# Optimization experiments

Hardware: AMD Instinct MI355X
Metric: run time of the kernel (lower is better)

The kernel has to match this reference:

```python
import jax, jax.numpy as jnp
import numpy as np

B, T, D, H = 4, 2048, 1024, 16
DK = DV = 64
R = 64
KS = 4
EPS = 1e-6


def setup_inputs() -> dict:
    key = jax.random.key(0)
    ks = jax.random.split(key, 16)
    def w(k, shape, s=0.02):
        return jax.random.normal(k, shape, jnp.float32) * s
    return {
        "x": jax.random.normal(ks[0], (B, T, D), jnp.float32),
        "conv_q_w": w(ks[1], (D, 1, KS), 0.3), "conv_q_b": jnp.zeros((D,), jnp.float32),
        "conv_k_w": w(ks[2], (D, 1, KS), 0.3), "conv_k_b": jnp.zeros((D,), jnp.float32),
        "conv_v_w": w(ks[3], (D, 1, KS), 0.3), "conv_v_b": jnp.zeros((D,), jnp.float32),
        "Wq": w(ks[4], (D, H * DK)), "bq": jnp.zeros((H * DK,), jnp.float32),
        "Wk": w(ks[5], (D, H * DK)), "bk": jnp.zeros((H * DK,), jnp.float32),
        "Wv": w(ks[6], (D, H * DV)), "bv": jnp.zeros((H * DV,), jnp.float32),
        "W_ad": w(ks[7], (D, R)), "b_ad": jnp.zeros((R,), jnp.float32),
        "W_au": w(ks[8], (R, H * DK)), "b_au": jnp.zeros((H * DK,), jnp.float32),
        "W_beta": w(ks[9], (D, H)), "b_beta": jnp.zeros((H,), jnp.float32),
        "rms_w": jnp.ones((H, DV), jnp.float32),
        "W_gd": w(ks[10], (D, R)), "b_gd": jnp.zeros((R,), jnp.float32),
        "W_gu": w(ks[11], (R, H)), "b_gu": jnp.zeros((H,), jnp.float32),
        "Wo": w(ks[12], (H * DV, D)), "bo": jnp.zeros((D,), jnp.float32),
    }


def _shortconv(x, w, b):
    # causal depthwise conv1d: torch pads (KS-1) both sides then slices [:T] == left-pad KS-1
    xc = jnp.transpose(x, (0, 2, 1))  # [B, D, T]
    y = jax.lax.conv_general_dilated(
        xc, w, (1,), [(KS - 1, 0)],
        dimension_numbers=("NCH", "OIH", "NCH"), feature_group_count=D)
    y = y + b[None, :, None]
    return jax.nn.silu(jnp.transpose(y, (0, 2, 1)))  # [B, T, D]


def _l2(x):
    # x / sqrt(clamp(sum(x^2), eps))  (matches torch clamp_min then sqrt)
    return x / jnp.sqrt(jnp.maximum(jnp.sum(x * x, -1, keepdims=True), EPS))


def _heads(z, dh):
    # [B,T,H*dh] -> [B*H,T,dh]
    return jnp.transpose(z.reshape(B, T, H, dh), (0, 2, 1, 3)).reshape(B * H, T, dh)


def reference(x, conv_q_w, conv_q_b, conv_k_w, conv_k_b, conv_v_w, conv_v_b,
              Wq, bq, Wk, bk, Wv, bv, W_ad, b_ad, W_au, b_au, W_beta, b_beta,
              rms_w, W_gd, b_gd, W_gu, b_gu, Wo, bo):
    qx = _shortconv(x, conv_q_w, conv_q_b)
    kx = _shortconv(x, conv_k_w, conv_k_b)
    vx = _shortconv(x, conv_v_w, conv_v_b)
    Q = _l2(_heads(qx @ Wq + bq, DK))            # [BH,T,DK]
    K = _l2(_heads(kx @ Wk + bk, DK))            # [BH,T,DK]
    V = _heads(vx @ Wv + bv, DV)                 # [BH,T,DV]
    alpha = jax.nn.sigmoid(jax.nn.silu(x @ W_ad + b_ad) @ W_au + b_au)  # [B,T,H*DK]
    A = _heads(alpha, DK)                        # [BH,T,DK]
    beta = jax.nn.sigmoid(x @ W_beta + b_beta)   # [B,T,H]
    Bta = jnp.transpose(beta, (0, 2, 1)).reshape(B * H, T, 1)

    S0 = jnp.zeros((B * H, DK, DV), jnp.float32)

    def step(S, inp):
        q, k, v, a, b = inp                      # [BH,DK],[BH,DK],[BH,DV],[BH,DK],[BH,1]
        S = S * a[:, :, None]                    # gated decay (row scale)
        kTS = jnp.einsum("bi,bij->bj", k, S)    # k^T S : [BH,DV]
        S = S + (b * k)[:, :, None] * (v - kTS)[:, None, :]  # rank-1 delta update
        o = jnp.einsum("bij,bi->bj", S, q)      # S^T q : [BH,DV]
        return S, o

    tm = lambda z: jnp.transpose(z, (1, 0, 2))   # time-major for scan
    S_final, out_t = jax.lax.scan(step, S0, (tm(Q), tm(K), tm(V), tm(A), tm(Bta)))
    O = jnp.transpose(out_t, (1, 0, 2)).reshape(B, H, T, DV)

    # headwise RMSNorm then sigmoid output gate
    var = jnp.mean(O * O, -1, keepdims=True)
    O = O * jax.lax.rsqrt(var + EPS) * rms_w[None, :, None, :]
    gate = jax.nn.sigmoid(jax.nn.silu(x @ W_gd + b_gd) @ W_gu + b_gu)  # [B,T,H]
    O = O * jnp.transpose(gate, (0, 2, 1))[:, :, :, None]

    y = jnp.transpose(O, (0, 2, 1, 3)).reshape(B, T, H * DV) @ Wo + bo
    return y, S_final.reshape(B, H, DK, DV)
```

## Files before the change

### kernel.cpp

```cpp
#include <hip/hip_runtime.h>
#include <hip/hip_bf16.h>
#include <cstdint>

#define BB 4
#define TT 2048
#define DD 1024
#define HH 16
#define NR (BB*TT)
#define CC 16
#define NCH (TT/CC)

typedef __attribute__((ext_vector_type(8))) short bf16x8;
typedef __attribute__((ext_vector_type(4))) float f32x4;
typedef __attribute__((ext_vector_type(2))) float f32x2;
typedef __attribute__((ext_vector_type(4))) unsigned int u32x4;
typedef __attribute__((ext_vector_type(2))) unsigned int u32x2;

#define GLL(g, l, SZ) __builtin_amdgcn_global_load_lds( \
    (const __attribute__((address_space(1))) void*)(uintptr_t)(const void*)(g), \
    (__attribute__((address_space(3))) void*)(uintptr_t)(void*)(l), SZ, 0, 0)

__device__ __forceinline__ unsigned short f2bf(float f) {
  unsigned u = __builtin_bit_cast(unsigned, f);
  unsigned r = 0x7FFFu + ((u >> 16) & 1u);
  return (unsigned short)((u + r) >> 16);
}
__device__ __forceinline__ unsigned pk2(float a, float b) {
  return (unsigned)f2bf(a) | ((unsigned)f2bf(b) << 16);
}
__device__ __forceinline__ float siluf(float v) { return v / (1.f + __expf(-v)); }
__device__ __forceinline__ float sigmf(float v) { return 1.f / (1.f + __expf(-v)); }


__global__ __launch_bounds__(256) void transpose_convert(
    const float* __restrict__ W, unsigned short* __restrict__ Wt, int K, int N) {
  __shared__ float tile[64][65];
  const int tid = threadIdx.x;
  const int bk = blockIdx.x * 64, bn = blockIdx.y * 64;
  const int r = tid >> 2, c4 = (tid & 3) * 16;
#pragma unroll 4
  for (int e = 0; e < 16; ++e)
    tile[r][c4 + e] = W[(size_t)(bk + r) * N + bn + c4 + e];
  __syncthreads();
#pragma unroll 4
  for (int e = 0; e < 16; ++e)
    Wt[(size_t)(bn + r) * K + bk + c4 + e] = f2bf(tile[c4 + e][r]);
}

__global__ void conv_small_T(const float* __restrict__ W, unsigned short* __restrict__ Wt,
                             int K, int N, int Npad) {
  int idx = blockIdx.x * 256 + threadIdx.x;
  if (idx >= Npad * K) return;
  int n = idx / K, k = idx - n * K;
  float v = (n < N) ? W[(size_t)k * N + n] : 0.f;
  Wt[idx] = f2bf(v);
}

__global__ void pack_stage1_T(const float* __restrict__ Wad, const float* __restrict__ Wgd,
                              const float* __restrict__ Wbeta, unsigned short* __restrict__ Wt) {
  int idx = blockIdx.x * 256 + threadIdx.x;
  int n = idx >> 10, k = idx & 1023;
  float v = 0.f;
  if (n < 64) v = Wad[(size_t)k * 64 + n];
  else if (n < 128) v = Wgd[(size_t)k * 64 + (n - 64)];
  else if (n < 144) v = Wbeta[(size_t)k * 16 + (n - 128)];
  Wt[idx] = f2bf(v);
}

__global__ void pack_bias(const float* __restrict__ bad, const float* __restrict__ bgd,
                          const float* __restrict__ bbeta, const float* __restrict__ bgu,
                          float* __restrict__ bst1, float* __restrict__ bgup) {
  int t = threadIdx.x;
  float v = 0.f;
  if (t < 64) v = bad[t];
  else if (t < 128) v = bgd[t - 64];
  else if (t < 144) v = bbeta[t - 128];
  bst1[t] = v;
  if (t < 128) bgup[t] = (t < 16) ? bgu[t] : 0.f;
}

__global__ __launch_bounds__(256) void conv_silu(
    const float* __restrict__ x,
    const float* __restrict__ qw, const float* __restrict__ qb,
    const float* __restrict__ kw, const float* __restrict__ kb,
    const float* __restrict__ vw, const float* __restrict__ vb,
    unsigned short* __restrict__ qx, unsigned short* __restrict__ kx,
    unsigned short* __restrict__ vx, unsigned short* __restrict__ xb) {
  const int n = blockIdx.x;
  const int t = n & (TT - 1);
  const int d0 = threadIdx.x * 4;
  const size_t base = (size_t)n * DD + d0;
  f32x4 zero = {0.f, 0.f, 0.f, 0.f};
  f32x4 x0 = *(const f32x4*)(x + base);
  f32x4 xm1 = (t >= 1) ? *(const f32x4*)(x + base - DD) : zero;
  f32x4 xm2 = (t >= 2) ? *(const f32x4*)(x + base - 2 * DD) : zero;
  f32x4 xm3 = (t >= 3) ? *(const f32x4*)(x + base - 3 * DD) : zero;
  float sq[4], sk[4], sv[4];
#pragma unroll
  for (int e = 0; e < 4; ++e) {
    const int d = d0 + e;
    const f32x4 wq = *(const f32x4*)(qw + (size_t)d * 4);
    const f32x4 wk = *(const f32x4*)(kw + (size_t)d * 4);
    const f32x4 wv = *(const f32x4*)(vw + (size_t)d * 4);
    float aq = wq[0] * xm3[e] + wq[1] * xm2[e] + wq[2] * xm1[e] + wq[3] * x0[e] + qb[d];
    float ak = wk[0] * xm3[e] + wk[1] * xm2[e] + wk[2] * xm1[e] + wk[3] * x0[e] + kb[d];
    float av = wv[0] * xm3[e] + wv[1] * xm2[e] + wv[2] * xm1[e] + wv[3] * x0[e] + vb[d];
    sq[e] = siluf(aq); sk[e] = siluf(ak); sv[e] = siluf(av);
  }
  u32x2 o;
  o[0] = pk2(sq[0], sq[1]); o[1] = pk2(sq[2], sq[3]); *(u32x2*)(qx + base) = o;
  o[0] = pk2(sk[0], sk[1]); o[1] = pk2(sk[2], sk[3]); *(u32x2*)(kx + base) = o;
  o[0] = pk2(sv[0], sv[1]); o[1] = pk2(sv[2], sv[3]); *(u32x2*)(vx + base) = o;
  o[0] = pk2(x0[0], x0[1]); o[1] = pk2(x0[2], x0[3]); *(u32x2*)(xb + base) = o;
}

template <int ACT>
__global__ __launch_bounds__(256) void gemm_bt(
    const unsigned short* __restrict__ A, const unsigned short* __restrict__ Bt,
    const float* __restrict__ bias, float* __restrict__ C,
    int M, int N, int K, int ldc, int nstore) {
  __shared__ unsigned short lsA[128 * 32];
  __shared__ unsigned short lsB[128 * 32];
  const int tid = threadIdx.x;
  const int wid = tid >> 6, lane = tid & 63;
  const int wr = wid >> 1, wc = wid & 1;
  const int m0 = blockIdx.x * 128, n0 = blockIdx.y * 128;
  f32x4 acc[4][4] = {};
  const int nk = K >> 5;
  const int r0 = wid * 32 + (lane >> 2);
  const int cb = (lane & 3) * 16;
  char* lA = (char*)lsA;
  char* lB = (char*)lsB;
  const size_t rowb = (size_t)K * 2;

  for (int kt = 0; kt < nk; ++kt) {
    const char* gA = (const char*)(A + (size_t)(m0 + r0) * K) + kt * 64 + cb;
    const char* gB = (const char*)(Bt + (size_t)(n0 + r0) * K) + kt * 64 + cb;
    GLL(gA, lA + (wid * 32) * 64, 16);
    GLL(gA + 16 * rowb, lA + (wid * 32 + 16) * 64, 16);
    GLL(gB, lB + (wid * 32) * 64, 16);
    GLL(gB + 16 * rowb, lB + (wid * 32 + 16) * 64, 16);
    __syncthreads();
    bf16x8 af[4], bfr[4];
#pragma unroll
    for (int f = 0; f < 4; ++f)
      af[f] = *(const bf16x8*)(lA + (wr * 64 + f * 16 + (lane & 15)) * 64 + (lane >> 4) * 16);
#pragma unroll
    for (int f = 0; f < 4; ++f)
      bfr[f] = *(const bf16x8*)(lB + (wc * 64 + f * 16 + (lane & 15)) * 64 + (lane >> 4) * 16);
#pragma unroll
    for (int i = 0; i < 4; ++i)
#pragma unroll
      for (int j = 0; j < 4; ++j)
        acc[i][j] = __builtin_amdgcn_mfma_f32_16x16x32_bf16(af[i], bfr[j], acc[i][j], 0, 0, 0);
    __syncthreads();
  }
#pragma unroll
  for (int i = 0; i < 4; ++i) {
    const int gr0 = m0 + wr * 64 + i * 16 + (lane >> 4) * 4;
#pragma unroll
    for (int j = 0; j < 4; ++j) {
      const int gc = n0 + wc * 64 + j * 16 + (lane & 15);
      if (gc < nstore) {
        const float bv = bias[gc];
#pragma unroll
        for (int r = 0; r < 4; ++r) {
          float v = acc[i][j][r] + bv;
          if (ACT == 1) v = sigmf(v);
          C[(size_t)(gr0 + r) * ldc + gc] = v;
        }
      }
    }
  }
}

__global__ __launch_bounds__(256) void l2norm_rows(float* __restrict__ Q) {
  const int tid = threadIdx.x;
  const int row = blockIdx.x * 4 + (tid >> 6);
  const int lane = tid & 63;
  float* p = Q + (size_t)row * DD + lane * 16;
  f32x4 v[4];
  float ss = 0.f;
#pragma unroll
  for (int u = 0; u < 4; ++u) {
    v[u] = *(const f32x4*)(p + u * 4);
#pragma unroll
    for (int e = 0; e < 4; ++e) ss = fmaf(v[u][e], v[u][e], ss);
  }
  ss += __shfl_xor(ss, 1);
  ss += __shfl_xor(ss, 2);
  const float rs = 1.f / sqrtf(fmaxf(ss, 1e-6f));
#pragma unroll
  for (int u = 0; u < 4; ++u) {
    f32x4 o;
#pragma unroll
    for (int e = 0; e < 4; ++e) o[e] = v[u][e] * rs;
    *(f32x4*)(p + u * 4) = o;
  }
}

__global__ void prep(const float* __restrict__ s1, unsigned short* __restrict__ ad,
                     unsigned short* __restrict__ gd, float* __restrict__ betaT) {
  const int n = blockIdx.x, t = threadIdx.x;
  float v = s1[(size_t)n * 256 + t];
  if (t < 64) ad[(size_t)n * 64 + t] = f2bf(siluf(v));
  else gd[(size_t)n * 64 + (t - 64)] = f2bf(siluf(v));
  if (t < 16) {
    float b = s1[(size_t)n * 256 + 128 + t];
    int bb = n >> 11, tt = n & (TT - 1);
    betaT[((size_t)(bb * HH + t)) * TT + tt] = sigmf(b);
  }
}

__global__ __launch_bounds__(256) void scan_phaseA(
    float* __restrict__ Qn, float* __restrict__ Kn, float* __restrict__ Vv,
    float* __restrict__ Alp, const float* __restrict__ betaT,
    float* __restrict__ Pbuf, float* __restrict__ bCbuf) {
  __shared__ float bA[CC][68], bKt[CC][68], bKp[CC][68], bQ[CC][68];
  __shared__ float bW1[CC][68], bW2[CC][68], bU1[CC][68], bU2[CC][68];
  __shared__ float Nm[CC][20], Nt[CC][20];
  __shared__ float bet[CC];
  const int bid = (int)blockIdx.x;
  const int bh = bid >> 7, c = bid & 127;
  const int b = bh >> 4, h = bh & 15;
  const int tid = threadIdx.x;
  const int tG = tid >> 4, sA = tid & 15, dG = sA * 4;
  const size_t seg = ((size_t)b * TT) * DD + h * 64;
  const size_t off = seg + (size_t)(c * CC + tG) * DD + dG;

  *(f32x4*)&bA [tG][dG] = *(const f32x4*)(Alp + off);
  *(f32x4*)&bKt[tG][dG] = *(const f32x4*)(Kn  + off);
  *(f32x4*)&bW1[tG][dG] = *(const f32x4*)(Vv  + off);
  *(f32x4*)&bQ [tG][dG] = *(const f32x4*)(Qn  + off);
  if (tid < CC) bet[tid] = betaT[(size_t)bh * TT + c * CC + tid];
  __syncthreads();

  if (tid < 64) {
    float p = bA[0][tid];
#pragma unroll
    for (int t = 1; t < CC; ++t) { p *= bA[t][tid]; bA[t][tid] = p; }
  }
  __syncthreads();

  {
    f32x4 bb = *(f32x4*)&bA[tG][dG];
    f32x4 kk = *(f32x4*)&bKt[tG][dG];
    f32x4 qq = *(f32x4*)&bQ[tG][dG];
    f32x4 vv = *(f32x4*)&bW1[tG][dG];
    f32x4 bC = *(f32x4*)&bA[CC - 1][dG];
    const float bt = bet[tG];
    f32x4 kt, kp, qt, w1, w2, kb;
#pragma unroll
    for (int e = 0; e < 4; ++e) {
      float inv = 1.0f / bb[e];
      kt[e] = kk[e] * bb[e];
      kp[e] = kk[e] * inv;
      qt[e] = qq[e] * bb[e];
      w1[e] = bt * vv[e];
      w2[e] = bt * kt[e];
      kb[e] = kp[e] * bC[e];
    }
    *(f32x4*)&bKt[tG][dG] = kt;
    *(f32x4*)&bKp[tG][dG] = kp;
    *(f32x4*)&bQ [tG][dG] = qt;
    *(f32x4*)&bW1[tG][dG] = w1;
    *(f32x4*)&bW2[tG][dG] = w2;
    *(f32x4*)(Qn + off) = qt;
    *(f32x4*)(Alp + off) = kb;
    if (tid < 64) bCbuf[((size_t)bh * 128 + c) * 64 + tid] = bA[CC - 1][tid];
  }
  __syncthreads();

  {
    f32x4 da = {0.f, 0.f, 0.f, 0.f}, dp = {0.f, 0.f, 0.f, 0.f};
#pragma unroll
    for (int ii = 0; ii < 16; ++ii) {
      f32x4 y = *(f32x4*)&bKp[sA][ii * 4];
      da += (*(f32x4*)&bKt[tG][ii * 4]) * y;
      dp += (*(f32x4*)&bQ [tG][ii * 4]) * y;
    }
    float dotA = (da[0] + da[1]) + (da[2] + da[3]);
    float dotP = (dp[0] + dp[1]) + (dp[2] + dp[3]);
    Nm[tG][sA] = (sA < tG) ? (-bet[tG] * dotA) : 0.f;
    Pbuf[((size_t)bh * 128 + c) * 256 + tG * 16 + sA] = (sA <= tG) ? dotP : 0.f;
  }
  __syncthreads();

#define NEUM2(Pw, I1, I2, O1, O2)                                        \
    {                                                                    \
      f32x4 a1 = *(f32x4*)&I1[tG][dG];                                   \
      f32x4 a2 = *(f32x4*)&I2[tG][dG];                                   \
      for (int s4 = 0; s4 < 4; ++s4) {                                   \
        f32x4 pv = *(f32x4*)&Pw[tG][s4 * 4];                             \
        _Pragma("unroll")                                                \
        for (int e = 0; e < 4; ++e) {                                    \
          a1 += pv[e] * (*(f32x4*)&I1[s4 * 4 + e][dG]);                  \
          a2 += pv[e] * (*(f32x4*)&I2[s4 * 4 + e][dG]);                  \
        }                                                                \
      }                                                                  \
      *(f32x4*)&O1[tG][dG] = a1;                                         \
      *(f32x4*)&O2[tG][dG] = a2;                                         \
    }
#define SQMAT(Pw, Pout)                                                  \
    {                                                                    \
      float acc = 0.f;                                                   \
      _Pragma("unroll")                                                  \
      for (int s = 0; s < 16; ++s) acc = fmaf(Pw[tG][s], Pw[s][sA], acc);\
      Pout[tG][sA] = acc;                                                \
    }

  NEUM2(Nm, bW1, bW2, bU1, bU2)
  SQMAT(Nm, Nt)
  __syncthreads();
  NEUM2(Nt, bU1, bU2, bW1, bW2)
  SQMAT(Nt, Nm)
  __syncthreads();
  NEUM2(Nm, bW1, bW2, bU1, bU2)
  SQMAT(Nm, Nt)
  __syncthreads();
  {
    f32x4 a1 = *(f32x4*)&bU1[tG][dG];
    f32x4 a2 = *(f32x4*)&bU2[tG][dG];
    for (int s4 = 0; s4 < 4; ++s4) {
      f32x4 pv = *(f32x4*)&Nt[tG][s4 * 4];
#pragma unroll
      for (int e = 0; e < 4; ++e) {
        a1 += pv[e] * (*(f32x4*)&bU1[s4 * 4 + e][dG]);
        a2 += pv[e] * (*(f32x4*)&bU2[s4 * 4 + e][dG]);
      }
    }
    *(f32x4*)(Vv + off) = a1;
    *(f32x4*)(Kn + off) = a2;
  }
#undef NEUM2
#undef SQMAT
}

__global__ __launch_bounds__(512, 2) void scan_phaseB(
    const float* __restrict__ W1g, const float* __restrict__ W2g,
    const float* __restrict__ Qt, const float* __restrict__ Kb,
    const float* __restrict__ Pbuf, const float* __restrict__ bCbuf,
    float* __restrict__ O, float* __restrict__ Sout) {
  __shared__ float S0[64][17];
  __shared__ float pU[2][16][17];
  __shared__ float pOq[2][16][17];
  __shared__ float pw2[2][16][68];
  __shared__ float pqt[2][16][68];
  __shared__ float pkb[2][16][68];
  __shared__ float pP [2][16][20];
  __shared__ float pbC[2][64];
  const int blk = (int)blockIdx.x;
  const int bh = blk >> 2, cg = blk & 3;
  const int b = bh >> 4, hh = bh & 15;
  const int tid = threadIdx.x;
  const int h = tid >> 8;
  const int t8 = tid & 255;
  const int T = t8 >> 4, j = t8 & 15;
  const int jg = cg * 16 + j;
  const size_t seg = ((size_t)b * TT) * DD + hh * 64;

  const int qr = t8 >> 4, qc = t8 & 15;

#define PLOAD(c, W2R, QTR, KBR, PR, BCR, W1R)                               \
  {                                                                         \
    const size_t rb = seg + (size_t)((c) * CC + qr) * DD + qc * 4;          \
    if (h == 0) {                                                           \
      W2R = *(const f32x4*)(W2g + rb);                                      \
      QTR = *(const f32x4*)(Qt + rb);                                       \
      W1R = W1g[seg + (size_t)((c) * CC + T) * DD + jg];                    \
    } else {                                                                \
      KBR = *(const f32x4*)(Kb + rb);                                       \
      PR  = Pbuf[((size_t)bh * 128 + (c)) * 256 + t8];                      \
      BCR = (t8 < 64) ? bCbuf[((size_t)bh * 128 + (c)) * 64 + t8] : 0.f;    \
    }                                                                       \
  }
#define PSTORE(bufI, W2R, QTR, KBR, PR, BCR)                                \
  {                                                                         \
    if (h == 0) {                                                           \
      *(f32x4*)&pw2[bufI][qr][qc * 4] = W2R;                                \
      *(f32x4*)&pqt[bufI][qr][qc * 4] = QTR;                                \
    } else {                                                                \
      *(f32x4*)&pkb[bufI][qr][qc * 4] = KBR;                                \
      pP[bufI][qr][qc] = PR;                                                \
      if (t8 < 64) pbC[bufI][t8] = BCR;                                     \
    }                                                                       \
  }

  f32x4 w2r = {}, qtr = {}, kbr = {};
  float pr = 0.f, bcr = 0.f, w1l = 0.f;
  PLOAD(0, w2r, qtr, kbr, pr, bcr, w1l)
  PSTORE(0, w2r, qtr, kbr, pr, bcr)
  {
    int e0 = tid, e1 = tid + 512;
    S0[e0 >> 4][e0 & 15] = 0.f;
    S0[e1 >> 4][e1 & 15] = 0.f;
  }
  __syncthreads();

  for (int c = 0; c < NCH; ++c) {
    const int buf = c & 1;
    f32x4 w2n = {}, qtn = {}, kbn = {};
    float pn = 0.f, bcn = 0.f, w1n = 0.f;
    const bool more = (c + 1 < NCH);
    if (more) PLOAD(c + 1, w2n, qtn, kbn, pn, bcn, w1n)

    float u0 = (h == 0) ? w1l : 0.f, u1 = 0.f, q0 = 0.f, q1 = 0.f;
#pragma unroll
    for (int k4 = 0; k4 < 8; ++k4) {
      const int kk = h * 32 + k4 * 4;
      f32x4 wv = *(const f32x4*)&pw2[buf][T][kk];
      f32x4 qv = *(const f32x4*)&pqt[buf][T][kk];
      float s0 = S0[kk + 0][j], s1 = S0[kk + 1][j];
      float s2 = S0[kk + 2][j], s3 = S0[kk + 3][j];
      u0 = fmaf(-wv[0], s0, u0); q0 = fmaf(qv[0], s0, q0);
      u1 = fmaf(-wv[1], s1, u1); q1 = fmaf(qv[1], s1, q1);
      u0 = fmaf(-wv[2], s2, u0); q0 = fmaf(qv[2], s2, q0);
      u1 = fmaf(-wv[3], s3, u1); q1 = fmaf(qv[3], s3, q1);
    }
    pU[h][T][j] = u0 + u1;
    pOq[h][T][j] = q0 + q1;
    __syncthreads();

    float um[CC];
#pragma unroll
    for (int s = 0; s < CC; ++s) um[s] = pU[0][s][j] + pU[1][s][j];

    if (h == 0) {
      float o = pOq[0][T][j] + pOq[1][T][j];
#pragma unroll
      for (int s4 = 0; s4 < 4; ++s4) {
        f32x4 pv = *(const f32x4*)&pP[buf][T][s4 * 4];
        o = fmaf(pv[0], um[s4 * 4 + 0], o);
        o = fmaf(pv[1], um[s4 * 4 + 1], o);
        o = fmaf(pv[2], um[s4 * 4 + 2], o);
        o = fmaf(pv[3], um[s4 * 4 + 3], o);
      }
      O[seg + (size_t)(c * CC + T) * DD + jg] = o;
    }

    {
      const int r0 = 4 * T + 2 * h;
      f32x2 bcv = *(const f32x2*)&pbC[buf][r0];
      float sp0 = bcv[0] * S0[r0 + 0][j];
      float sp1 = bcv[1] * S0[r0 + 1][j];
#pragma unroll
      for (int s = 0; s < CC; ++s) {
        f32x2 kv = *(const f32x2*)&pkb[buf][s][r0];
        sp0 = fmaf(kv[0], um[s], sp0);
        sp1 = fmaf(kv[1], um[s], sp1);
      }
      S0[r0 + 0][j] = sp0;
      S0[r0 + 1][j] = sp1;
    }

    if (more) PSTORE(buf ^ 1, w2n, qtn, kbn, pn, bcn)
    __syncthreads();
    w1l = w1n;
  }
#undef PLOAD
#undef PSTORE

  {
    const int r0 = 4 * T + 2 * h;
    Sout[(size_t)bh * 4096 + (size_t)(r0 + 0) * 64 + jg] = S0[r0 + 0][j];
    Sout[(size_t)bh * 4096 + (size_t)(r0 + 1) * 64 + jg] = S0[r0 + 1][j];
  }
}

__global__ __launch_bounds__(256) void rms_gate(
    const float* __restrict__ O, const float* __restrict__ rmsw,
    const float* __restrict__ gate, unsigned short* __restrict__ Og) {
  const int tid = threadIdx.x;
  const int row = blockIdx.x * 4 + (tid >> 6);
  const int lane = tid & 63;
  const int h = lane >> 2;
  const float* p = O + (size_t)row * DD + lane * 16;
  f32x4 v[4];
  float ss = 0.f;
#pragma unroll
  for (int u = 0; u < 4; ++u) {
    v[u] = *(const f32x4*)(p + u * 4);
#pragma unroll
    for (int e = 0; e < 4; ++e) ss = fmaf(v[u][e], v[u][e], ss);
  }
  ss += __shfl_xor(ss, 1);
  ss += __shfl_xor(ss, 2);
  const float rs = rsqrtf(ss * (1.f / 64.f) + 1e-6f);
  const float g = gate[row * 16 + h];
  const float* wp = rmsw + h * 64 + (lane & 3) * 16;
  unsigned ow[8];
#pragma unroll
  for (int u = 0; u < 4; ++u) {
    f32x4 wv = *(const f32x4*)(wp + u * 4);
    float a0 = v[u][0] * rs * wv[0] * g, a1 = v[u][1] * rs * wv[1] * g;
    float a2 = v[u][2] * rs * wv[2] * g, a3 = v[u][3] * rs * wv[3] * g;
    ow[u * 2] = pk2(a0, a1);
    ow[u * 2 + 1] = pk2(a2, a3);
  }
  u32x4* dst = (u32x4*)(Og + (size_t)row * DD + lane * 16);
  u32x4 o1, o2;
  o1[0] = ow[0]; o1[1] = ow[1]; o1[2] = ow[2]; o1[3] = ow[3];
  o2[0] = ow[4]; o2[1] = ow[5]; o2[2] = ow[6]; o2[3] = ow[7];
  dst[0] = o1; dst[1] = o2;
}

extern "C" void kernel_launch(void* const* d_in, const int* in_sizes, int n_in,
                              void* d_out, int out_size, void* d_ws, size_t ws_size,
                              hipStream_t stream) {
  const float* x    = (const float*)d_in[0];
  const float* qw   = (const float*)d_in[1];
  const float* qb   = (const float*)d_in[2];
  const float* kw   = (const float*)d_in[3];
  const float* kb   = (const float*)d_in[4];
  const float* vw   = (const float*)d_in[5];
  const float* vb   = (const float*)d_in[6];
  const float* Wq   = (const float*)d_in[7];
  const float* bq   = (const float*)d_in[8];
  const float* Wk   = (const float*)d_in[9];
  const float* bk   = (const float*)d_in[10];
  const float* Wv   = (const float*)d_in[11];
  const float* bv   = (const float*)d_in[12];
  const float* Wad  = (const float*)d_in[13];
  const float* bad  = (const float*)d_in[14];
  const float* Wau  = (const float*)d_in[15];
  const float* bau  = (const float*)d_in[16];
  const float* Wbeta= (const float*)d_in[17];
  const float* bbeta= (const float*)d_in[18];
  const float* rmsw = (const float*)d_in[19];
  const float* Wgd  = (const float*)d_in[20];
  const float* bgd  = (const float*)d_in[21];
  const float* Wgu  = (const float*)d_in[22];
  const float* bgu  = (const float*)d_in[23];
  const float* Wo   = (const float*)d_in[24];
  const float* bo   = (const float*)d_in[25];

  char* ws = (char*)d_ws;
  const size_t MB = 1ull << 20;
  unsigned short* WqT   = (unsigned short*)(ws + 0 * MB);
  unsigned short* WkT   = (unsigned short*)(ws + 2 * MB);
  unsigned short* WvT   = (unsigned short*)(ws + 4 * MB);
  unsigned short* WoT   = (unsigned short*)(ws + 6 * MB);
  unsigned short* WauT  = (unsigned short*)(ws + 8 * MB);
  unsigned short* Wst1T = (unsigned short*)(ws + 8 * MB + 256 * 1024);
  unsigned short* WguT  = (unsigned short*)(ws + 8 * MB + 768 * 1024);
  float* bst1 = (float*)(ws + 8 * MB + 800 * 1024);
  float* bgup = (float*)(ws + 8 * MB + 804 * 1024);
  unsigned short* x_bf = (unsigned short*)(ws + 9 * MB);
  unsigned short* qx   = (unsigned short*)(ws + 25 * MB);
  unsigned short* kx   = (unsigned short*)(ws + 41 * MB);
  unsigned short* vx   = (unsigned short*)(ws + 57 * MB);
  float* Qn    = (float*)(ws + 73 * MB);
  float* Kn    = (float*)(ws + 105 * MB);
  float* Vv    = (float*)(ws + 137 * MB);
  float* stage1= (float*)(ws + 169 * MB);
  unsigned short* adb = (unsigned short*)(ws + 177 * MB);
  unsigned short* gdb = (unsigned short*)(ws + 178 * MB);
  float* betaT = (float*)(ws + 179 * MB);
  float* gate  = (float*)(ws + 179 * MB + 512 * 1024);
  float* bCbuf = (float*)(ws + 180 * MB);
  float* alpha = (float*)(ws + 9 * MB);
  float* Obuf  = (float*)(ws + 41 * MB);
  unsigned short* Og = (unsigned short*)(ws + 137 * MB);
  float* Pbuf  = stage1;
  float* y = (float*)d_out;
  float* Sout = y + (size_t)NR * DD;

  dim3 blk(256);
  transpose_convert<<<dim3(16, 16), blk, 0, stream>>>(Wq, WqT, 1024, 1024);
  transpose_convert<<<dim3(16, 16), blk, 0, stream>>>(Wk, WkT, 1024, 1024);
  transpose_convert<<<dim3(16, 16), blk, 0, stream>>>(Wv, WvT, 1024, 1024);
  transpose_convert<<<dim3(16, 16), blk, 0, stream>>>(Wo, WoT, 1024, 1024);
  conv_small_T<<<dim3(256), blk, 0, stream>>>(Wau, WauT, 64, 1024, 1024);
  pack_stage1_T<<<dim3(1024), blk, 0, stream>>>(Wad, Wgd, Wbeta, Wst1T);
  conv_small_T<<<dim3(32), blk, 0, stream>>>(Wgu, WguT, 64, 16, 128);
  pack_bias<<<dim3(1), blk, 0, stream>>>(bad, bgd, bbeta, bgu, bst1, bgup);

  conv_silu<<<dim3(NR), blk, 0, stream>>>(x, qw, qb, kw, kb, vw, vb, qx, kx, vx, x_bf);

  gemm_bt<0><<<dim3(64, 2), blk, 0, stream>>>(x_bf, Wst1T, bst1, stage1, NR, 256, 1024, 256, 256);
  gemm_bt<0><<<dim3(64, 8), blk, 0, stream>>>(qx, WqT, bq, Qn, NR, 1024, 1024, 1024, 1024);
  gemm_bt<0><<<dim3(64, 8), blk, 0, stream>>>(kx, WkT, bk, Kn, NR, 1024, 1024, 1024, 1024);
  gemm_bt<0><<<dim3(64, 8), blk, 0, stream>>>(vx, WvT, bv, Vv, NR, 1024, 1024, 1024, 1024);
  l2norm_rows<<<dim3(2048), blk, 0, stream>>>(Qn);
  l2norm_rows<<<dim3(2048), blk, 0, stream>>>(Kn);
  prep<<<dim3(NR), dim3(128), 0, stream>>>(stage1, adb, gdb, betaT);
  gemm_bt<1><<<dim3(64, 8), blk, 0, stream>>>(adb, WauT, bau, alpha, NR, 1024, 64, 1024, 1024);
  gemm_bt<1><<<dim3(64, 1), blk, 0, stream>>>(gdb, WguT, bgup, gate, NR, 128, 64, 16, 16);

  scan_phaseA<<<dim3(8192), blk, 0, stream>>>(Qn, Kn, Vv, alpha, betaT, Pbuf, bCbuf);
  scan_phaseB<<<dim3(256), dim3(512), 0, stream>>>(Vv, Kn, Qn, alpha, Pbuf, bCbuf, Obuf, Sout);

  rms_gate<<<dim3(2048), blk, 0, stream>>>(Obuf, rmsw, gate, Og);
  gemm_bt<0><<<dim3(64, 8), blk, 0, stream>>>(Og, WoT, bo, y, NR, 1024, 1024, 1024, 1024);
}
```

Baseline: 542.6 us.

## Fuse per-head L2 norm into Q/K GEMM epilogue and swizzle blocks across XCDs

Adds an epilogue mode to the bf16 GEMM that adds the bias, computes each row's per-head sum of squares via lane shuffles, and writes L2-normalised Q and K directly. This removes the two separate l2norm passes and their extra global read/write of the Q and K buffers. It also remaps workgroup indices in chunks of 8 so that neighbouring tiles land on the same XCD, aiming for better L2 reuse. The epilogue relies on each warp's 64-column tile aligning exactly with one head.

```diff
diff --git a/kernel.cpp b/kernel.cpp
--- a/kernel.cpp
+++ b/kernel.cpp
@@ -124,7 +124,18 @@
   const int tid = threadIdx.x;
   const int wid = tid >> 6, lane = tid & 63;
   const int wr = wid >> 1, wc = wid & 1;
-  const int m0 = blockIdx.x * 128, n0 = blockIdx.y * 128;
+  int bx = blockIdx.x, by = blockIdx.y;
+  {
+    const int nwg = gridDim.x * gridDim.y;
+    if ((nwg & 7) == 0) {
+      const int flat = by * gridDim.x + bx;
+      const int cpx = nwg >> 3;
+      const int nf = (flat & 7) * cpx + (flat >> 3);
+      bx = nf % gridDim.x;
+      by = nf / gridDim.x;
+    }
+  }
+  const int m0 = bx * 128, n0 = by * 128;
   f32x4 acc[4][4] = {};
   const int nk = K >> 5;
   const int r0 = wid * 32 + (lane >> 2);
@@ -155,6 +166,43 @@
         acc[i][j] = __builtin_amdgcn_mfma_f32_16x16x32_bf16(af[i], bfr[j], acc[i][j], 0, 0, 0);
     __syncthreads();
   }
+
+  if (ACT == 2) {
+#pragma unroll
+    for (int i = 0; i < 4; ++i) {
+      float ss[4] = {0.f, 0.f, 0.f, 0.f};
+#pragma unroll
+      for (int j = 0; j < 4; ++j) {
+        const int gc = n0 + wc * 64 + j * 16 + (lane & 15);
+        const float bv = bias[gc];
+#pragma unroll
+        for (int r = 0; r < 4; ++r) {
+          float v = acc[i][j][r] + bv;
+          acc[i][j][r] = v;
+          ss[r] = fmaf(v, v, ss[r]);
+        }
+      }
+#pragma unroll
+      for (int r = 0; r < 4; ++r) {
+        float s = ss[r];
+        s += __shfl_xor(s, 1);
+        s += __shfl_xor(s, 2);
+        s += __shfl_xor(s, 4);
+        s += __shfl_xor(s, 8);
+        ss[r] = 1.f / sqrtf(fmaxf(s, 1e-6f));
+      }
+      const int gr0 = m0 + wr * 64 + i * 16 + (lane >> 4) * 4;
+#pragma unroll
+      for (int j = 0; j < 4; ++j) {
+        const int gc = n0 + wc * 64 + j * 16 + (lane & 15);
+#pragma unroll
+        for (int r = 0; r < 4; ++r)
+          C[(size_t)(gr0 + r) * ldc + gc] = acc[i][j][r] * ss[r];
+      }
+    }
+    return;
+  }
+
 #pragma unroll
   for (int i = 0; i < 4; ++i) {
     const int gr0 = m0 + wr * 64 + i * 16 + (lane >> 4) * 4;
@@ -171,31 +219,6 @@
         }
       }
     }
-  }
-}
-
-__global__ __launch_bounds__(256) void l2norm_rows(float* __restrict__ Q) {
-  const int tid = threadIdx.x;
-  const int row = blockIdx.x * 4 + (tid >> 6);
-  const int lane = tid & 63;
-  float* p = Q + (size_t)row * DD + lane * 16;
-  f32x4 v[4];
-  float ss = 0.f;
-#pragma unroll
-  for (int u = 0; u < 4; ++u) {
-    v[u] = *(const f32x4*)(p + u * 4);
-#pragma unroll
-    for (int e = 0; e < 4; ++e) ss = fmaf(v[u][e], v[u][e], ss);
-  }
-  ss += __shfl_xor(ss, 1);
-  ss += __shfl_xor(ss, 2);
-  const float rs = 1.f / sqrtf(fmaxf(ss, 1e-6f));
-#pragma unroll
-  for (int u = 0; u < 4; ++u) {
-    f32x4 o;
-#pragma unroll
-    for (int e = 0; e < 4; ++e) o[e] = v[u][e] * rs;
-    *(f32x4*)(p + u * 4) = o;
   }
 }
 
@@ -578,11 +601,9 @@
   conv_silu<<<dim3(NR), blk, 0, stream>>>(x, qw, qb, kw, kb, vw, vb, qx, kx, vx, x_bf);
 
   gemm_bt<0><<<dim3(64, 2), blk, 0, stream>>>(x_bf, Wst1T, bst1, stage1, NR, 256, 1024, 256, 256);
-  gemm_bt<0><<<dim3(64, 8), blk, 0, stream>>>(qx, WqT, bq, Qn, NR, 1024, 1024, 1024, 1024);
-  gemm_bt<0><<<dim3(64, 8), blk, 0, stream>>>(kx, WkT, bk, Kn, NR, 1024, 1024, 1024, 1024);
+  gemm_bt<2><<<dim3(64, 8), blk, 0, stream>>>(qx, WqT, bq, Qn, NR, 1024, 1024, 1024, 1024);
+  gemm_bt<2><<<dim3(64, 8), blk, 0, stream>>>(kx, WkT, bk, Kn, NR, 1024, 1024, 1024, 1024);
   gemm_bt<0><<<dim3(64, 8), blk, 0, stream>>>(vx, WvT, bv, Vv, NR, 1024, 1024, 1024, 1024);
-  l2norm_rows<<<dim3(2048), blk, 0, stream>>>(Qn);
-  l2norm_rows<<<dim3(2048), blk, 0, stream>>>(Kn);
   prep<<<dim3(NR), dim3(128), 0, stream>>>(stage1, adb, gdb, betaT);
   gemm_bt<1><<<dim3(64, 8), blk, 0, stream>>>(adb, WauT, bau, alpha, NR, 1024, 64, 1024, 1024);
   gemm_bt<1><<<dim3(64, 1), blk, 0, stream>>>(gdb, WguT, bgup, gate, NR, 128, 64, 16, 16);
```

Result: faster. 520.2 us (-4.1%).
